# Optimization experiments

Measured on AMD Instinct MI355X. Metric: run time of the kernel, lower is better.

Reference implementation:

```python
import jax, jax.numpy as jnp
from jax import lax
import numpy as np

D_MODEL, D_STATE, D_CONV, EXPAND = 256, 16, 4, 2
D_INNER = EXPAND * D_MODEL            # 512
DT_RANK = (D_MODEL + 15) // 16        # 16
B, NVAR, SEG = 4, 32, 96


def _mamba_params(key, scale=0.02):
    ks = jax.random.split(key, 7)
    in_w = jax.random.normal(ks[0], (2 * D_INNER, D_MODEL)) * scale
    conv_w = jax.random.normal(ks[1], (D_INNER, D_CONV)) * scale
    conv_b = jnp.zeros((D_INNER,))
    xproj_w = jax.random.normal(ks[2], (DT_RANK + 2 * D_STATE, D_INNER)) * scale
    dt_w = jax.random.normal(ks[3], (D_INNER, DT_RANK)) * scale
    # bias so softplus(dt_b) ~ dt in [1e-3, 1e-1] (mamba-style init)
    dt = jnp.exp(jax.random.uniform(ks[4], (D_INNER,)) * (np.log(0.1) - np.log(1e-3)) + np.log(1e-3))
    dt_b = dt + jnp.log(-jnp.expm1(-dt))  # inverse softplus
    A_log = jnp.log(jnp.broadcast_to(jnp.arange(1, D_STATE + 1, dtype=jnp.float32), (D_INNER, D_STATE)))
    Dvec = jnp.ones((D_INNER,))
    out_w = jax.random.normal(ks[5], (D_MODEL, D_INNER)) * scale
    return in_w, conv_w, conv_b, xproj_w, dt_w, dt_b, A_log, Dvec, out_w


def setup_inputs() -> dict:
    key = jax.random.key(0)
    kx, kt, kd = jax.random.split(key, 3)
    x = jax.random.normal(kx, (B, NVAR, SEG, D_MODEL), dtype=jnp.float32)
    t = _mamba_params(kt)
    d = _mamba_params(kd)
    names = ["in_w", "conv_w", "conv_b", "xproj_w", "dt_w", "dt_b", "A_log", "D", "out_w"]
    inp = {"x": x}
    inp.update({f"t_{n}": v for n, v in zip(names, t)})
    inp.update({f"d_{n}": v for n, v in zip(names, d)})
    return inp


def _mamba(x, in_w, conv_w, conv_b, xproj_w, dt_w, dt_b, A_log, Dvec, out_w):
    # x: [Bn, L, d_model] -> [Bn, L, d_model]
    Bn, L, _ = x.shape
    xz = jnp.einsum("bld,ed->ble", x, in_w)          # [Bn, L, 2*d_inner]
    xi, z = jnp.split(xz, 2, axis=-1)
    # causal depthwise conv over time
    xi_nc = xi.transpose(0, 2, 1)                     # [Bn, d_inner, L]
    xc = lax.conv_general_dilated(xi_nc, conv_w[:, None, :], (1,),
                                  [(D_CONV - 1, 0)], feature_group_count=D_INNER)
    xc = jax.nn.silu(xc + conv_b[None, :, None]).transpose(0, 2, 1)  # [Bn, L, d_inner]
    dbl = jnp.einsum("ble,fe->blf", xc, xproj_w)      # [Bn, L, dt_rank+2*d_state]
    dt, Bm, Cm = jnp.split(dbl, [DT_RANK, DT_RANK + D_STATE], axis=-1)
    dt = jax.nn.softplus(jnp.einsum("blr,er->ble", dt, dt_w) + dt_b)  # [Bn, L, d_inner]
    A = -jnp.exp(A_log)                               # [d_inner, d_state]

    def step(h, inp):
        dt_t, B_t, C_t, u_t = inp                     # [Bn,dI], [Bn,dS], [Bn,dS], [Bn,dI]
        dA = jnp.exp(dt_t[:, :, None] * A)            # [Bn, d_inner, d_state]
        h = dA * h + dt_t[:, :, None] * B_t[:, None, :] * u_t[:, :, None]
        y = jnp.einsum("bes,bs->be", h, C_t)
        return h, y

    h0 = jnp.zeros((Bn, D_INNER, D_STATE), x.dtype)
    _, ys = lax.scan(step, h0, (dt.transpose(1, 0, 2), Bm.transpose(1, 0, 2),
                                Cm.transpose(1, 0, 2), xc.transpose(1, 0, 2)))
    y = ys.transpose(1, 0, 2) + xc * Dvec             # skip term D*u
    y = y * jax.nn.silu(z)                            # gate
    return jnp.einsum("ble,de->bld", y, out_w)


def reference(x,
              t_in_w, t_conv_w, t_conv_b, t_xproj_w, t_dt_w, t_dt_b, t_A_log, t_D, t_out_w,
              d_in_w, d_conv_w, d_conv_b, d_xproj_w, d_dt_w, d_dt_b, d_A_log, d_D, d_out_w):
    Bb, Dv, S, dm = x.shape
    # stage 1: time-wise scan per variable
    xt = _mamba(x.reshape(Bb * Dv, S, dm),
                t_in_w, t_conv_w, t_conv_b, t_xproj_w, t_dt_w, t_dt_b, t_A_log, t_D, t_out_w)
    xt = xt.reshape(Bb, Dv, S, dm)
    # stage 2: dimension-wise scan per time segment
    xd = _mamba(xt.transpose(0, 2, 1, 3).reshape(Bb * S, Dv, dm),
                d_in_w, d_conv_w, d_conv_b, d_xproj_w, d_dt_w, d_dt_b, d_A_log, d_D, d_out_w)
    return xd.reshape(Bb, S, Dv, dm).transpose(0, 2, 1, 3)
```

## Files before the change

kernel.cpp:

```cpp
#include <hip/hip_runtime.h>
#include <hip/hip_bf16.h>
#include <math.h>

#define D_MODEL 256
#define D_STATE 16
#define D_INNER 512
#define DT_RANK 16
#define NB 4
#define NVAR 32
#define SEG 96
#define TOKENS (NB*NVAR*SEG)

typedef float f4 __attribute__((ext_vector_type(4)));

__device__ __forceinline__ float silu_f(float x) { return x / (1.0f + __expf(-x)); }

__global__ __launch_bounds__(256)
void transpose_w(const float* __restrict__ W, float* __restrict__ WT, int N, int K)
{
    __shared__ float t[32][33];
    const int k0 = blockIdx.x * 32, n0 = blockIdx.y * 32;
    const int tx = threadIdx.x & 31, ty = threadIdx.x >> 5;
#pragma unroll
    for (int i = 0; i < 32; i += 8)
        t[ty + i][tx] = W[(size_t)(n0 + ty + i) * K + k0 + tx];
    __syncthreads();
#pragma unroll
    for (int i = 0; i < 32; i += 8)
        WT[(size_t)(k0 + ty + i) * N + n0 + tx] = t[tx][ty + i];
}

template<int K, int BN, int BK, int MODE>
__global__ __launch_bounds__(256, 4)
void gemm_v6(const float* __restrict__ A, const float* __restrict__ WT,
             float* __restrict__ C, int N)
{
    constexpr int NT  = K / BK;
    constexpr int CPL = BN / 64;
    constexpr int KRD = 1024 / (BN * 4);
    constexpr int J   = BK / (KRD * 4);
    typedef float cvec __attribute__((ext_vector_type(CPL)));
    __shared__ float wlds[2 * BK * BN];

    const int tid  = threadIdx.x;
    const int lane = tid & 63;
    const int wid  = __builtin_amdgcn_readfirstlane(tid >> 6);
    const int m0 = blockIdx.x * 32;
    const int n0 = blockIdx.y * BN;

    const float* Ar[8];
#pragma unroll
    for (int r = 0; r < 8; r++)
        Ar[r] = A + (size_t)(m0 + wid * 8 + r) * K;

    auto stage = [&](int dbuf, int k0) {
#pragma unroll
        for (int j = 0; j < J; j++) {
            int kb   = (wid * J + j) * KRD;
            int krow = kb + ((KRD == 2) ? (lane >> 5) : 0);
            int nofs = ((KRD == 2) ? (lane & 31) : lane) * 4;
            int dstw = __builtin_amdgcn_readfirstlane(dbuf * (BK * BN) + kb * BN);
            __builtin_amdgcn_global_load_lds(
                (const __attribute__((address_space(1))) void*)
                    (WT + (size_t)(k0 + krow) * N + n0 + nofs),
                (__attribute__((address_space(3))) void*)(wlds + dstw), 16, 0, 0);
        }
    };

    float acc[8][CPL];
#pragma unroll
    for (int r = 0; r < 8; r++)
#pragma unroll
        for (int g = 0; g < CPL; g++) acc[r][g] = 0.0f;

    stage(0, 0);
    __syncthreads();

    for (int t = 0; t < NT; t++) {
        const int k0 = t * BK;
        if (t + 1 < NT) stage((t + 1) & 1, k0 + BK);
        const float* Wb = wlds + (t & 1) * (BK * BN);
#pragma unroll
        for (int q = 0; q < BK / 4; q++) {
            f4 a4[8];
#pragma unroll
            for (int r = 0; r < 8; r++)
                a4[r] = *(const f4*)(Ar[r] + k0 + 4 * q);
#pragma unroll
            for (int e = 0; e < 4; e++) {
                cvec wv = *(const cvec*)(Wb + (4 * q + e) * BN + CPL * lane);
#pragma unroll
                for (int r = 0; r < 8; r++)
#pragma unroll
                    for (int g = 0; g < CPL; g++)
                        acc[r][g] = fmaf(a4[r][e], wv[g], acc[r][g]);
            }
        }
        __syncthreads();
    }

#pragma unroll
    for (int r = 0; r < 8; r++) {
        int m = m0 + wid * 8 + r;
        int orow = m;
        if (MODE == 2) {
            int b = m / 3072, rr = m % 3072;
            int v = rr / 96, s = rr % 96;
            orow = (b * 96 + s) * 32 + v;
        } else if (MODE == 3) {
            int b = m / 3072, rr = m % 3072;
            int s = rr / 32, v = rr % 32;
            orow = (b * 32 + v) * 96 + s;
        }
        cvec v;
#pragma unroll
        for (int g = 0; g < CPL; g++) v[g] = acc[r][g];
        *(cvec*)(C + (size_t)orow * N + n0 + CPL * lane) = v;
    }
}

__global__ __launch_bounds__(256)
void xproj_dt(const float* __restrict__ xc,
              const float* __restrict__ xpw,
              const float* __restrict__ dtw,
              const float* __restrict__ dtb,
              float* __restrict__ dbl,
              float* __restrict__ dty,
              int M)
{
    constexpr int BM = 32, BN = 64, BK = 32, TM = 2, TN = 4;
    __shared__ float As[BK][BM + 4];
    __shared__ float Ws[BK][BN + 4];
    __shared__ float dbl_s[BM][52];

    const int tid = threadIdx.x;
    const int tx  = tid % (BN / TN);
    const int ty  = tid / (BN / TN);
    const int m0  = blockIdx.x * BM;

    float acc[TM][TN];
#pragma unroll
    for (int i = 0; i < TM; i++)
#pragma unroll
        for (int j = 0; j < TN; j++) acc[i][j] = 0.0f;

    constexpr int AF4 = (BM * BK) / 1024;
    constexpr int WF4 = (BN * BK) / 1024;
    constexpr int F4R = BK / 4;

    for (int k0 = 0; k0 < 512; k0 += BK) {
#pragma unroll
        for (int c = 0; c < AF4; c++) {
            int idx = tid + c * 256;
            int row = idx / F4R;
            int kc  = (idx % F4R) * 4;
            float4 v = *(const float4*)(xc + (size_t)(m0 + row) * 512 + k0 + kc);
            As[kc + 0][row] = v.x;
            As[kc + 1][row] = v.y;
            As[kc + 2][row] = v.z;
            As[kc + 3][row] = v.w;
        }
#pragma unroll
        for (int c = 0; c < WF4; c++) {
            int idx = tid + c * 256;
            int row = idx / F4R;
            int kc  = (idx % F4R) * 4;
            float4 v;
            if (row < 48) v = *(const float4*)(xpw + (size_t)row * 512 + k0 + kc);
            else          v = make_float4(0.f, 0.f, 0.f, 0.f);
            Ws[kc + 0][row] = v.x;
            Ws[kc + 1][row] = v.y;
            Ws[kc + 2][row] = v.z;
            Ws[kc + 3][row] = v.w;
        }
        __syncthreads();

#pragma unroll
        for (int kk = 0; kk < BK; kk++) {
            float a[TM], w[TN];
#pragma unroll
            for (int i = 0; i < TM; i++) a[i] = As[kk][ty * TM + i];
#pragma unroll
            for (int j = 0; j < TN; j++) w[j] = Ws[kk][tx * TN + j];
#pragma unroll
            for (int i = 0; i < TM; i++)
#pragma unroll
                for (int j = 0; j < TN; j++)
                    acc[i][j] = fmaf(a[i], w[j], acc[i][j]);
        }
        __syncthreads();
    }

#pragma unroll
    for (int i = 0; i < TM; i++) {
        int mr = ty * TM + i;
#pragma unroll
        for (int j = 0; j < TN; j++) {
            int n = tx * TN + j;
            if (n < 48) {
                dbl[(size_t)(m0 + mr) * 48 + n] = acc[i][j];
                dbl_s[mr][n] = acc[i][j];
            }
        }
    }
    __syncthreads();

    f4 wA[4], wB[4];
#pragma unroll
    for (int c = 0; c < 4; c++) {
        wA[c] = *(const f4*)(dtw + (size_t)tid * 16 + 4 * c);
        wB[c] = *(const f4*)(dtw + (size_t)(tid + 256) * 16 + 4 * c);
    }
    const float bA = dtb[tid], bB = dtb[tid + 256];
#pragma unroll 4
    for (int r = 0; r < BM; r++) {
        f4 d[4];
#pragma unroll
        for (int c = 0; c < 4; c++) d[c] = *(const f4*)(&dbl_s[r][4 * c]);
        float vA = bA, vB = bB;
#pragma unroll
        for (int c = 0; c < 4; c++)
#pragma unroll
            for (int e = 0; e < 4; e++) {
                vA = fmaf(d[c][e], wA[c][e], vA);
                vB = fmaf(d[c][e], wB[c][e], vB);
            }
        vA = (vA > 20.0f) ? vA : log1pf(__expf(vA));
        vB = (vB > 20.0f) ? vB : log1pf(__expf(vB));
        dty[(size_t)(m0 + r) * 512 + tid]       = vA;
        dty[(size_t)(m0 + r) * 512 + tid + 256] = vB;
    }
}

__global__ __launch_bounds__(256)
void conv_silu(const float* __restrict__ xz, const float* __restrict__ cw,
               const float* __restrict__ cb, float* __restrict__ xc, int L)
{
    int i = blockIdx.x * 256 + threadIdx.x;
    int e = i % D_INNER;
    int t = i / D_INNER;
    int l = t % L;
    float acc = cb[e];
#pragma unroll
    for (int j = 0; j < 4; j++) {
        int li = l - 3 + j;
        if (li >= 0) acc = fmaf(xz[(size_t)(t + li - l) * 1024 + e], cw[e * 4 + j], acc);
    }
    xc[i] = silu_f(acc);
}

__global__ __launch_bounds__(256)
void scan_gate4(float* __restrict__ dty,
                const float* __restrict__ xc,
                const float* __restrict__ xz,
                const float* __restrict__ dbl,
                const float* __restrict__ A_log,
                const float* __restrict__ Dvec,
                int L)
{
    int bn = blockIdx.x >> 3;
    int e  = ((blockIdx.x & 7) << 6) + (threadIdx.x >> 2);
    int sh = (threadIdx.x & 3) << 2;

    float Ae[4], h[4];
#pragma unroll
    for (int s = 0; s < 4; s++) {
        Ae[s] = -__expf(A_log[e * D_STATE + sh + s]);
        h[s]  = 0.0f;
    }
    const float De = Dvec[e];

    const int base = bn * L;
    const int last = base + L - 1;

#define LOADS(tk, dt_, u_, B_, C_, z_)                                  \
    dt_ = dty[(size_t)(tk) * 512 + e];                                  \
    u_  = xc [(size_t)(tk) * 512 + e];                                  \
    B_  = *(const f4*)(dbl + (size_t)(tk) * 48 + 16 + sh);              \
    C_  = *(const f4*)(dbl + (size_t)(tk) * 48 + 32 + sh);              \
    z_  = xz [(size_t)(tk) * 1024 + 512 + e];

#define COMPUTE(tk, dt_, u_, B_, C_, z_)                                \
    {                                                                   \
        float y = 0.0f;                                                 \
        _Pragma("unroll")                                               \
        for (int s = 0; s < 4; s++) {                                   \
            float dA = __expf((dt_) * Ae[s]);                           \
            h[s] = fmaf(dA, h[s], (dt_) * (B_)[s] * (u_));              \
            y    = fmaf(h[s], (C_)[s], y);                              \
        }                                                               \
        y += __shfl_xor(y, 1);                                          \
        y += __shfl_xor(y, 2);                                          \
        if (sh == 0)                                                    \
            dty[(size_t)(tk) * 512 + e] = (y + (u_) * De) * silu_f(z_); \
    }

    float dt0, u0, z0, dt1, u1, z1;
    f4 B0, C0, B1, C1;
    LOADS(base, dt0, u0, B0, C0, z0);
    LOADS(base + 1, dt1, u1, B1, C1, z1);

    for (int l = 0; l < L; l += 2) {
        int tk = base + l;
        COMPUTE(tk, dt0, u0, B0, C0, z0);
        {
            int tp = tk + 2 > last ? last : tk + 2;
            LOADS(tp, dt0, u0, B0, C0, z0);
        }
        COMPUTE(tk + 1, dt1, u1, B1, C1, z1);
        {
            int tp = tk + 3 > last ? last : tk + 3;
            LOADS(tp, dt1, u1, B1, C1, z1);
        }
    }
#undef LOADS
#undef COMPUTE
}

template<int OUTMODE>
static void run_stage(const float* xin,
                      const float* in_wT, const float* conv_w, const float* conv_b,
                      const float* xproj_w, const float* dt_w, const float* dt_b,
                      const float* A_log, const float* Dvec, const float* out_wT,
                      float* xz, float* xc, float* dbl, float* dty, float* outp,
                      int Bn, int L, hipStream_t stream)
{
    const int M = TOKENS;
    gemm_v6<256, 256, 16, 0><<<dim3(M / 32, 1024 / 256), 256, 0, stream>>>(xin, in_wT, xz, 1024);
    conv_silu<<<dim3((M * D_INNER) / 256), 256, 0, stream>>>(xz, conv_w, conv_b, xc, L);
    xproj_dt<<<dim3(M / 32), 256, 0, stream>>>(xc, xproj_w, dt_w, dt_b, dbl, dty, M);
    scan_gate4<<<dim3(Bn * 8), 256, 0, stream>>>(dty, xc, xz, dbl, A_log, Dvec, L);
    gemm_v6<512, 128, 32, OUTMODE><<<dim3(M / 32, 256 / 128), 256, 0, stream>>>(dty, out_wT, outp, 256);
}

extern "C" void kernel_launch(void* const* d_in, const int* in_sizes, int n_in,
                              void* d_out, int out_size, void* d_ws, size_t ws_size,
                              hipStream_t stream)
{
    const float* x = (const float*)d_in[0];
    const float* t_in_w    = (const float*)d_in[1];
    const float* t_conv_w  = (const float*)d_in[2];
    const float* t_conv_b  = (const float*)d_in[3];
    const float* t_xproj_w = (const float*)d_in[4];
    const float* t_dt_w    = (const float*)d_in[5];
    const float* t_dt_b    = (const float*)d_in[6];
    const float* t_A_log   = (const float*)d_in[7];
    const float* t_D       = (const float*)d_in[8];
    const float* t_out_w   = (const float*)d_in[9];
    const float* d_in_w    = (const float*)d_in[10];
    const float* d_conv_w  = (const float*)d_in[11];
    const float* d_conv_b  = (const float*)d_in[12];
    const float* d_xproj_w = (const float*)d_in[13];
    const float* d_dt_w    = (const float*)d_in[14];
    const float* d_dt_b    = (const float*)d_in[15];
    const float* d_A_log   = (const float*)d_in[16];
    const float* d_D       = (const float*)d_in[17];
    const float* d_out_w   = (const float*)d_in[18];

    float* ws  = (float*)d_ws;
    float* xz  = ws;
    float* xc  = xz  + (size_t)TOKENS * 1024;
    float* dbl = xc  + (size_t)TOKENS * 512;
    float* dty = dbl + (size_t)TOKENS * 48;
    float* xt  = dty + (size_t)TOKENS * 512;
    float* t_in_wT  = xt + (size_t)TOKENS * 256;
    float* t_out_wT = t_in_wT  + 262144;
    float* d_in_wT  = t_out_wT + 131072;
    float* d_out_wT = d_in_wT  + 262144;
    const size_t need_bytes =
        ((size_t)TOKENS * (1024 + 512 + 48 + 512 + 256) + 2 * (262144 + 131072)) * 4;
    if (ws_size < need_bytes) return;

    transpose_w<<<dim3(256 / 32, 1024 / 32), 256, 0, stream>>>(t_in_w,  t_in_wT,  1024, 256);
    transpose_w<<<dim3(512 / 32,  256 / 32), 256, 0, stream>>>(t_out_w, t_out_wT,  256, 512);
    transpose_w<<<dim3(256 / 32, 1024 / 32), 256, 0, stream>>>(d_in_w,  d_in_wT,  1024, 256);
    transpose_w<<<dim3(512 / 32,  256 / 32), 256, 0, stream>>>(d_out_w, d_out_wT,  256, 512);

    run_stage<2>(x, t_in_wT, t_conv_w, t_conv_b, t_xproj_w, t_dt_w, t_dt_b,
                 t_A_log, t_D, t_out_wT, xz, xc, dbl, dty, xt,
                 NB * NVAR, SEG, stream);
    run_stage<3>(xt, d_in_wT, d_conv_w, d_conv_b, d_xproj_w, d_dt_w, d_dt_b,
                 d_A_log, d_D, d_out_wT, xz, xc, dbl, dty, (float*)d_out,
                 NB * SEG, NVAR, stream);
}
```

Baseline: 513.0 us.

## Vectorize conv_silu, deepen scan prefetch to four steps, retile input GEMM

The depthwise conv kernel now handles four channels per thread, using float4 loads for inputs, weights and bias and a float4 store. This cuts the thread count and memory instruction count. The selective scan's software-pipelined prefetch goes from two to four in-flight timesteps, to hide more global load latency on the serial recurrence at the cost of extra registers. The input projection GEMM tile changes from N=256/K=16 to N=128/K=32, which doubles its grid in N. The conv kernel assumes L is a multiple of 4 in the scan loop; L=96 and 32 both satisfy this.

Result: faster. 494.9 us (-3.5%).

```diff
diff --git a/kernel.cpp b/kernel.cpp
--- a/kernel.cpp
+++ b/kernel.cpp
@@ -236,17 +236,30 @@
 void conv_silu(const float* __restrict__ xz, const float* __restrict__ cw,
                const float* __restrict__ cb, float* __restrict__ xc, int L)
 {
-    int i = blockIdx.x * 256 + threadIdx.x;
-    int e = i % D_INNER;
-    int t = i / D_INNER;
-    int l = t % L;
-    float acc = cb[e];
+    int i  = blockIdx.x * 256 + threadIdx.x;
+    int e4 = (i & 127) << 2;
+    int t  = i >> 7;
+    int l  = t % L;
+    const f4 w0 = *(const f4*)(cw + e4 * 4);
+    const f4 w1 = *(const f4*)(cw + e4 * 4 + 4);
+    const f4 w2 = *(const f4*)(cw + e4 * 4 + 8);
+    const f4 w3 = *(const f4*)(cw + e4 * 4 + 12);
+    f4 acc = *(const f4*)(cb + e4);
 #pragma unroll
     for (int j = 0; j < 4; j++) {
         int li = l - 3 + j;
-        if (li >= 0) acc = fmaf(xz[(size_t)(t + li - l) * 1024 + e], cw[e * 4 + j], acc);
-    }
-    xc[i] = silu_f(acc);
+        if (li >= 0) {
+            f4 xv = *(const f4*)(xz + (size_t)(t + li - l) * 1024 + e4);
+            acc[0] = fmaf(xv[0], w0[j], acc[0]);
+            acc[1] = fmaf(xv[1], w1[j], acc[1]);
+            acc[2] = fmaf(xv[2], w2[j], acc[2]);
+            acc[3] = fmaf(xv[3], w3[j], acc[3]);
+        }
+    }
+    f4 o;
+#pragma unroll
+    for (int c = 0; c < 4; c++) o[c] = silu_f(acc[c]);
+    *(f4*)(xc + (size_t)t * 512 + e4) = o;
 }
 
 __global__ __launch_bounds__(256)
@@ -295,26 +308,33 @@
             dty[(size_t)(tk) * 512 + e] = (y + (u_) * De) * silu_f(z_); \
     }
 
-    float dt0, u0, z0, dt1, u1, z1;
-    f4 B0, C0, B1, C1;
-    LOADS(base, dt0, u0, B0, C0, z0);
+#define REFILL(slot_tk, dt_, u_, B_, C_, z_)                            \
+    {                                                                   \
+        int tp = (slot_tk) > last ? last : (slot_tk);                   \
+        LOADS(tp, dt_, u_, B_, C_, z_);                                 \
+    }
+
+    float dt0, u0, z0, dt1, u1, z1, dt2, u2, z2, dt3, u3, z3;
+    f4 B0, C0, B1, C1, B2, C2, B3, C3;
+    LOADS(base,     dt0, u0, B0, C0, z0);
     LOADS(base + 1, dt1, u1, B1, C1, z1);
-
-    for (int l = 0; l < L; l += 2) {
+    LOADS(base + 2, dt2, u2, B2, C2, z2);
+    LOADS(base + 3, dt3, u3, B3, C3, z3);
+
+    for (int l = 0; l < L; l += 4) {
         int tk = base + l;
-        COMPUTE(tk, dt0, u0, B0, C0, z0);
-        {
-            int tp = tk + 2 > last ? last : tk + 2;
-            LOADS(tp, dt0, u0, B0, C0, z0);
-        }
+        COMPUTE(tk,     dt0, u0, B0, C0, z0);
+        REFILL(tk + 4,  dt0, u0, B0, C0, z0);
         COMPUTE(tk + 1, dt1, u1, B1, C1, z1);
-        {
-            int tp = tk + 3 > last ? last : tk + 3;
-            LOADS(tp, dt1, u1, B1, C1, z1);
-        }
+        REFILL(tk + 5,  dt1, u1, B1, C1, z1);
+        COMPUTE(tk + 2, dt2, u2, B2, C2, z2);
+        REFILL(tk + 6,  dt2, u2, B2, C2, z2);
+        COMPUTE(tk + 3, dt3, u3, B3, C3, z3);
+        REFILL(tk + 7,  dt3, u3, B3, C3, z3);
     }
 #undef LOADS
 #undef COMPUTE
+#undef REFILL
 }
 
 template<int OUTMODE>
@@ -326,8 +346,8 @@
                       int Bn, int L, hipStream_t stream)
 {
     const int M = TOKENS;
-    gemm_v6<256, 256, 16, 0><<<dim3(M / 32, 1024 / 256), 256, 0, stream>>>(xin, in_wT, xz, 1024);
-    conv_silu<<<dim3((M * D_INNER) / 256), 256, 0, stream>>>(xz, conv_w, conv_b, xc, L);
+    gemm_v6<256, 128, 32, 0><<<dim3(M / 32, 1024 / 128), 256, 0, stream>>>(xin, in_wT, xz, 1024);
+    conv_silu<<<dim3((M * 128) / 256), 256, 0, stream>>>(xz, conv_w, conv_b, xc, L);
     xproj_dt<<<dim3(M / 32), 256, 0, stream>>>(xc, xproj_w, dt_w, dt_b, dbl, dty, M);
     scan_gate4<<<dim3(Bn * 8), 256, 0, stream>>>(dty, xc, xz, dbl, A_log, Dvec, L);
     gemm_v6<512, 128, 32, OUTMODE><<<dim3(M / 32, 256 / 128), 256, 0, stream>>>(dty, out_wT, outp, 256);
```
